# Optimization experiments

Hardware: AMD Instinct MI355X
Metric: run time of the kernel (lower is better)

Reference implementation:

```python
import math
import jax, jax.numpy as jnp
import numpy as np

K = 8
D = 8
LAMBDA_PRIOR = 0.01
TRI = D * (D + 1) // 2  # 36
PHI_DIM = K + K * D + K * TRI  # 360
_ROWS, _COLS = np.tril_indices(D)


def _unpack_phi(phi):
    # phi: [M, PHI_DIM] -> pi_tilde [M,K], mu [M,K,D], L_vecs [M,K,TRI]
    M = phi.shape[0]
    pi_tilde = phi[:, :K]
    mu = phi[:, K:K + K * D].reshape(M, K, D)
    L_vecs = phi[:, K + K * D:].reshape(M, K, TRI)
    return pi_tilde, mu, L_vecs


def _L_vec_to_matrix(L_vecs):
    # L_vecs: [M,K,TRI] -> lower-triangular L [M,K,D,D]
    M, Kc, _ = L_vecs.shape
    L = jnp.zeros((M, Kc, D, D), dtype=L_vecs.dtype)
    return L.at[:, :, _ROWS, _COLS].set(L_vecs)


def _gmm_log_likelihood(phi, X):
    # phi: [M, PHI_DIM], X: [N, D] -> log_lik [M]
    pi_tilde, mu, L_vecs = _unpack_phi(phi)
    log_pi = jax.nn.log_softmax(pi_tilde, axis=-1)          # [M,K]
    L = _L_vec_to_matrix(L_vecs)                             # [M,K,D,D]
    diff = X[None, None, :, :] - mu[:, :, None, :]           # [M,K,N,D]
    diff_T = jnp.swapaxes(diff, -1, -2)                      # [M,K,D,N]
    # solve L alpha = diff_T for each (m,k); batched triangular solve
    alpha = jax.scipy.linalg.solve_triangular(L, diff_T, lower=True)  # [M,K,D,N]
    maha = jnp.sum(alpha * alpha, axis=-2)                   # [M,K,N]
    log_diag = jnp.log(jnp.clip(jnp.abs(jnp.diagonal(L, axis1=-2, axis2=-1)), 1e-8))
    log_det = 2.0 * jnp.sum(log_diag, axis=-1)               # [M,K]
    log_norm_const = -0.5 * (D * math.log(2 * math.pi) + log_det[:, :, None])
    log_gauss = log_norm_const - 0.5 * maha                  # [M,K,N]
    log_mix = jax.scipy.special.logsumexp(log_pi[:, :, None] + log_gauss, axis=1)  # [M,N]
    return jnp.sum(log_mix, axis=-1)                         # [M]


def setup_inputs() -> dict:
    key = jax.random.key(0)
    k1, k2 = jax.random.split(key)
    M, N = 32, 32768
    phi = jax.random.normal(k1, (M, PHI_DIM), dtype=jnp.float32)
    X = jax.random.normal(k2, (N, D), dtype=jnp.float32)
    return {"phi": phi, "X": X}


def reference(phi, X):
    # U(phi; X) = -log p(X|phi) + lambda_prior * ||phi||^2 / 2  -> [M]
    log_lik = _gmm_log_likelihood(phi, X)
    prior = 0.5 * jnp.sum(phi * phi, axis=-1)
    return -log_lik + LAMBDA_PRIOR * prior
```

## Files before the change

### kernel.cpp

```cpp
#include <hip/hip_runtime.h>
#include <math.h>

#define KK 8
#define DD 8
#define TRI 36
#define PHI_DIM 360
#define MM 32
#define NN 32768
#define GX 16
#define TPB 256
#define PP 4

__global__ void prior_kernel(const float* __restrict__ phi, float* __restrict__ out) {
    int m = blockIdx.x;
    const float* p = phi + m * PHI_DIM;
    float s = 0.f;
    for (int j = threadIdx.x; j < PHI_DIM; j += 64) {
        float v = p[j];
        s += v * v;
    }
    #pragma unroll
    for (int off = 32; off; off >>= 1) s += __shfl_down(s, off, 64);
    if (threadIdx.x == 0) out[m] = 0.01f * 0.5f * s;
}

__launch_bounds__(TPB)
__global__ void gmm_kernel(const float* __restrict__ phi, const float* __restrict__ X,
                           float* __restrict__ out) {
    __shared__ float s_mu[KK][DD];
    __shared__ float s_L[KK][TRI];
    __shared__ float s_c[KK];
    __shared__ float s_pi[KK];
    __shared__ float s_red[TPB / 64];

    const int m = blockIdx.y;
    const float* ph = phi + m * PHI_DIM;
    const int tid = threadIdx.x;

    if (tid < KK) {
        const int k = tid;
        s_pi[k] = ph[k];
        #pragma unroll
        for (int i = 0; i < DD; i++) s_mu[k][i] = ph[KK + k * DD + i];
        #pragma unroll
        for (int t = 0; t < TRI; t++) s_L[k][t] = ph[KK + KK * DD + k * TRI + t];
        float logdet = 0.f;
        #pragma unroll
        for (int i = 0; i < DD; i++) {
            const int di = i * (i + 1) / 2 + i;
            float dv = s_L[k][di];
            logdet += 2.f * logf(fmaxf(fabsf(dv), 1e-8f));
            s_L[k][di] = 1.f / dv;
        }
        s_c[k] = -0.5f * (8.f * 1.8378770664093453f + logdet);
    }
    __syncthreads();
    if (tid < KK) {
        float mx = s_pi[0];
        #pragma unroll
        for (int i = 1; i < KK; i++) mx = fmaxf(mx, s_pi[i]);
        float sum = 0.f;
        #pragma unroll
        for (int i = 0; i < KK; i++) sum += expf(s_pi[i] - mx);
        float lse = mx + logf(sum);
        s_c[tid] += s_pi[tid] - lse;
    }
    __syncthreads();

    float acc = 0.f;
    const int base0 = blockIdx.x * (NN / GX);
    #pragma unroll 1
    for (int pass = 0; pass < (NN / GX) / (TPB * PP); ++pass) {
        const int n0 = base0 + pass * TPB * PP + tid;

        float x[PP][DD];
        #pragma unroll
        for (int p = 0; p < PP; p++) {
            const float4* xp = (const float4*)(X + (size_t)(n0 + p * TPB) * DD);
            float4 u0 = xp[0], u1 = xp[1];
            x[p][0] = u0.x; x[p][1] = u0.y; x[p][2] = u0.z; x[p][3] = u0.w;
            x[p][4] = u1.x; x[p][5] = u1.y; x[p][6] = u1.z; x[p][7] = u1.w;
        }

        float mrun[PP], srun[PP];
        #pragma unroll
        for (int p = 0; p < PP; p++) { mrun[p] = -INFINITY; srun[p] = 0.f; }

        #pragma unroll
        for (int k = 0; k < KK; k++) {
            float mu[DD], L[TRI];
            #pragma unroll
            for (int i = 0; i < DD; i++) mu[i] = s_mu[k][i];
            #pragma unroll
            for (int t = 0; t < TRI; t++) L[t] = s_L[k][t];
            const float c = s_c[k];

            #pragma unroll
            for (int p = 0; p < PP; p++) {
                float a[DD];
                float maha = 0.f;
                #pragma unroll
                for (int i = 0; i < DD; i++) {
                    float t = x[p][i] - mu[i];
                    #pragma unroll
                    for (int j = 0; j < i; j++)
                        t = fmaf(-L[i * (i + 1) / 2 + j], a[j], t);
                    a[i] = t * L[i * (i + 1) / 2 + i];
                    maha = fmaf(a[i], a[i], maha);
                }
                const float v = c - 0.5f * maha;
                const float mnew = fmaxf(mrun[p], v);
                srun[p] = srun[p] * __expf(mrun[p] - mnew) + __expf(v - mnew);
                mrun[p] = mnew;
            }
        }
        #pragma unroll
        for (int p = 0; p < PP; p++) acc += mrun[p] + __logf(srun[p]);
    }

    #pragma unroll
    for (int off = 32; off; off >>= 1) acc += __shfl_down(acc, off, 64);
    if ((tid & 63) == 0) s_red[tid >> 6] = acc;
    __syncthreads();
    if (tid == 0) {
        float t = s_red[0] + s_red[1] + s_red[2] + s_red[3];
        atomicAdd(&out[m], -t);
    }
}

extern "C" void kernel_launch(void* const* d_in, const int* in_sizes, int n_in,
                              void* d_out, int out_size, void* d_ws, size_t ws_size,
                              hipStream_t stream) {
    const float* phi = (const float*)d_in[0];
    const float* X   = (const float*)d_in[1];
    float* out = (float*)d_out;

    prior_kernel<<<MM, 64, 0, stream>>>(phi, out);
    dim3 grid(GX, MM);
    gmm_kernel<<<grid, TPB, 0, stream>>>(phi, X, out);
}
```

Measured before the change: 83.21 us.

## Fuse prior into GMM kernel, double grid, replace online logsumexp with two-pass

Moves the prior computation into the main kernel (computed by blockIdx.x==0 blocks) and replaces the prior launch with a memset. It doubles the grid so each block handles one pass of points without a loop. It also packs the parameters into one shared array and swaps the per-component online logsumexp for storing all component values, then taking a max and sum of exps once. The aim is fewer exps and launches and better occupancy, at the cost of more registers for v[PP][KK].

```diff
diff --git a/kernel.cpp b/kernel.cpp
--- a/kernel.cpp
+++ b/kernel.cpp
@@ -7,124 +7,108 @@
 #define PHI_DIM 360
 #define MM 32
 #define NN 32768
-#define GX 16
+#define GX 32
 #define TPB 256
 #define PP 4
-
-__global__ void prior_kernel(const float* __restrict__ phi, float* __restrict__ out) {
-    int m = blockIdx.x;
-    const float* p = phi + m * PHI_DIM;
-    float s = 0.f;
-    for (int j = threadIdx.x; j < PHI_DIM; j += 64) {
-        float v = p[j];
-        s += v * v;
-    }
-    #pragma unroll
-    for (int off = 32; off; off >>= 1) s += __shfl_down(s, off, 64);
-    if (threadIdx.x == 0) out[m] = 0.01f * 0.5f * s;
-}
 
 __launch_bounds__(TPB)
 __global__ void gmm_kernel(const float* __restrict__ phi, const float* __restrict__ X,
                            float* __restrict__ out) {
-    __shared__ float s_mu[KK][DD];
-    __shared__ float s_L[KK][TRI];
-    __shared__ float s_c[KK];
-    __shared__ float s_pi[KK];
+    __shared__ float s_par[KK][48];
     __shared__ float s_red[TPB / 64];
 
     const int m = blockIdx.y;
-    const float* ph = phi + m * PHI_DIM;
+    const float* __restrict__ ph = phi + m * PHI_DIM;
     const int tid = threadIdx.x;
 
     if (tid < KK) {
         const int k = tid;
-        s_pi[k] = ph[k];
         #pragma unroll
-        for (int i = 0; i < DD; i++) s_mu[k][i] = ph[KK + k * DD + i];
+        for (int i = 0; i < DD; i++) s_par[k][i] = ph[KK + k * DD + i];
         #pragma unroll
-        for (int t = 0; t < TRI; t++) s_L[k][t] = ph[KK + KK * DD + k * TRI + t];
+        for (int t = 0; t < TRI; t++) s_par[k][8 + t] = ph[KK + KK * DD + k * TRI + t];
         float logdet = 0.f;
         #pragma unroll
         for (int i = 0; i < DD; i++) {
-            const int di = i * (i + 1) / 2 + i;
-            float dv = s_L[k][di];
-            logdet += 2.f * logf(fmaxf(fabsf(dv), 1e-8f));
-            s_L[k][di] = 1.f / dv;
+            const int di = 8 + i * (i + 1) / 2 + i;
+            float dv = s_par[k][di];
+            logdet += 2.f * __logf(fmaxf(fabsf(dv), 1e-8f));
+            s_par[k][di] = 1.f / dv;
         }
-        s_c[k] = -0.5f * (8.f * 1.8378770664093453f + logdet);
-    }
-    __syncthreads();
-    if (tid < KK) {
-        float mx = s_pi[0];
+        float mx = ph[0];
         #pragma unroll
-        for (int i = 1; i < KK; i++) mx = fmaxf(mx, s_pi[i]);
+        for (int i = 1; i < KK; i++) mx = fmaxf(mx, ph[i]);
         float sum = 0.f;
         #pragma unroll
-        for (int i = 0; i < KK; i++) sum += expf(s_pi[i] - mx);
-        float lse = mx + logf(sum);
-        s_c[tid] += s_pi[tid] - lse;
+        for (int i = 0; i < KK; i++) sum += __expf(ph[i] - mx);
+        const float lse = mx + __logf(sum);
+        s_par[k][44] = (ph[k] - lse) - 0.5f * (8.f * 1.8378770664093453f + logdet);
+    }
+
+    float pr = 0.f;
+    if (blockIdx.x == 0) {
+        for (int j = tid; j < PHI_DIM; j += TPB) {
+            float v = ph[j];
+            pr = fmaf(v, v, pr);
+        }
     }
     __syncthreads();
 
-    float acc = 0.f;
-    const int base0 = blockIdx.x * (NN / GX);
-    #pragma unroll 1
-    for (int pass = 0; pass < (NN / GX) / (TPB * PP); ++pass) {
-        const int n0 = base0 + pass * TPB * PP + tid;
+    const int n0 = blockIdx.x * (NN / GX) + tid;
+    float x[PP][DD];
+    #pragma unroll
+    for (int p = 0; p < PP; p++) {
+        const float4* xp = (const float4*)(X + (size_t)(n0 + p * TPB) * DD);
+        float4 u0 = xp[0], u1 = xp[1];
+        x[p][0] = u0.x; x[p][1] = u0.y; x[p][2] = u0.z; x[p][3] = u0.w;
+        x[p][4] = u1.x; x[p][5] = u1.y; x[p][6] = u1.z; x[p][7] = u1.w;
+    }
 
-        float x[PP][DD];
+    float v[PP][KK];
+    #pragma unroll
+    for (int k = 0; k < KK; k++) {
+        float par[45];
+        #pragma unroll
+        for (int t = 0; t < 45; t++) par[t] = s_par[k][t];
+
         #pragma unroll
         for (int p = 0; p < PP; p++) {
-            const float4* xp = (const float4*)(X + (size_t)(n0 + p * TPB) * DD);
-            float4 u0 = xp[0], u1 = xp[1];
-            x[p][0] = u0.x; x[p][1] = u0.y; x[p][2] = u0.z; x[p][3] = u0.w;
-            x[p][4] = u1.x; x[p][5] = u1.y; x[p][6] = u1.z; x[p][7] = u1.w;
+            float a[DD];
+            float maha = 0.f;
+            #pragma unroll
+            for (int i = 0; i < DD; i++) {
+                float t = x[p][i] - par[i];
+                #pragma unroll
+                for (int j = 0; j < i; j++)
+                    t = fmaf(-par[8 + i * (i + 1) / 2 + j], a[j], t);
+                a[i] = t * par[8 + i * (i + 1) / 2 + i];
+                maha = fmaf(a[i], a[i], maha);
+            }
+            v[p][k] = par[44] - 0.5f * maha;
         }
-
-        float mrun[PP], srun[PP];
-        #pragma unroll
-        for (int p = 0; p < PP; p++) { mrun[p] = -INFINITY; srun[p] = 0.f; }
-
-        #pragma unroll
-        for (int k = 0; k < KK; k++) {
-            float mu[DD], L[TRI];
-            #pragma unroll
-            for (int i = 0; i < DD; i++) mu[i] = s_mu[k][i];
-            #pragma unroll
-            for (int t = 0; t < TRI; t++) L[t] = s_L[k][t];
-            const float c = s_c[k];
-
-            #pragma unroll
-            for (int p = 0; p < PP; p++) {
-                float a[DD];
-                float maha = 0.f;
-                #pragma unroll
-                for (int i = 0; i < DD; i++) {
-                    float t = x[p][i] - mu[i];
-                    #pragma unroll
-                    for (int j = 0; j < i; j++)
-                        t = fmaf(-L[i * (i + 1) / 2 + j], a[j], t);
-                    a[i] = t * L[i * (i + 1) / 2 + i];
-                    maha = fmaf(a[i], a[i], maha);
-                }
-                const float v = c - 0.5f * maha;
-                const float mnew = fmaxf(mrun[p], v);
-                srun[p] = srun[p] * __expf(mrun[p] - mnew) + __expf(v - mnew);
-                mrun[p] = mnew;
-            }
-        }
-        #pragma unroll
-        for (int p = 0; p < PP; p++) acc += mrun[p] + __logf(srun[p]);
     }
 
+    float acc = 0.f;
     #pragma unroll
-    for (int off = 32; off; off >>= 1) acc += __shfl_down(acc, off, 64);
-    if ((tid & 63) == 0) s_red[tid >> 6] = acc;
+    for (int p = 0; p < PP; p++) {
+        float mx = v[p][0];
+        #pragma unroll
+        for (int i = 1; i < KK; i++) mx = fmaxf(mx, v[p][i]);
+        float s = 0.f;
+        #pragma unroll
+        for (int i = 0; i < KK; i++) s += __expf(v[p][i] - mx);
+        acc += mx + __logf(s);
+    }
+
+    float contrib = 0.005f * pr - acc;
+
+    #pragma unroll
+    for (int off = 32; off; off >>= 1) contrib += __shfl_down(contrib, off, 64);
+    if ((tid & 63) == 0) s_red[tid >> 6] = contrib;
     __syncthreads();
     if (tid == 0) {
         float t = s_red[0] + s_red[1] + s_red[2] + s_red[3];
-        atomicAdd(&out[m], -t);
+        atomicAdd(&out[m], t);
     }
 }
 
@@ -135,7 +119,7 @@
     const float* X   = (const float*)d_in[1];
     float* out = (float*)d_out;
 
-    prior_kernel<<<MM, 64, 0, stream>>>(phi, out);
+    hipMemsetAsync(out, 0, out_size * sizeof(float), stream);
     dim3 grid(GX, MM);
     gmm_kernel<<<grid, TPB, 0, stream>>>(phi, X, out);
 }
```

After: 72.10 us. 1.15x faster.
